# Optimization experiments

Hardware: AMD Instinct MI355X
Metric: run time of the kernel (lower is better)

The kernel has to match this reference:

```python
import jax, jax.numpy as jnp
import numpy as np

EPS = 1e-12  # matches torch.nn.functional.normalize default eps
TOP_K = 5


def _l2_normalize(x):
    n = jnp.linalg.norm(x, axis=-1, keepdims=True)
    return x / jnp.maximum(n, EPS)


def setup_inputs() -> dict:
    key = jax.random.key(0)
    k1, k2, k3 = jax.random.split(key, 3)
    B, S, D = 64, 128, 256
    CAP = 500000
    return {
        "query": jax.random.normal(k1, (B, S, D), dtype=jnp.float32),
        "memory_keys": jax.random.normal(k2, (CAP, D), dtype=jnp.float32),
        "memory_values": jax.random.normal(k3, (CAP, D), dtype=jnp.float32),
        "access_counts": jnp.zeros((CAP,), dtype=jnp.float32),
    }


def reference(query, memory_keys, memory_values, access_counts):
    # 3D query -> mean over sequence dim
    if query.ndim == 3:
        query = query.mean(axis=1)  # [B, D]
    q_norm = _l2_normalize(query)            # [B, D]
    k_norm = _l2_normalize(memory_keys)      # [CAP, D]
    sims = q_norm @ k_norm.T                 # [B, CAP] cosine similarities
    _, top_idx = jax.lax.top_k(sims, TOP_K)  # [B, 5]
    # gather top-k values and mean over k -> [B, D]
    retrieved = memory_values[top_idx].mean(axis=1)
    # scatter-add access counts (buffer side-effect in torch, returned here)
    new_counts = access_counts.at[top_idx.reshape(-1)].add(1.0)
    return retrieved, new_counts
```

## Files before the change

### kernel.cpp

```cpp
#include <hip/hip_runtime.h>
#include <math.h>

#define NQ    64
#define DIM   256
#define SEQ   128
#define CAP   500000
#define TOPK  5
#define KT    32
#define NTILE (CAP / KT)
#define NBLK  1024
#define PB    5
#define NC    (NBLK * PB)
#define DELTA 3.0e-3f
#define MAXC  192

typedef short short8v __attribute__((ext_vector_type(8)));
typedef float f32x4   __attribute__((ext_vector_type(4)));

#define SYNC_NODRAIN() do {                                        \
    asm volatile("s_waitcnt lgkmcnt(0)" ::: "memory");             \
    __builtin_amdgcn_s_barrier();                                  \
    asm volatile("" ::: "memory"); } while (0)

__device__ inline unsigned pkbf(float a, float b) {
    unsigned ua = __builtin_bit_cast(unsigned, a);
    unsigned ub = __builtin_bit_cast(unsigned, b);
    ua = (ua + 0x7fffu + ((ua >> 16) & 1u)) >> 16;
    ub = (ub + 0x7fffu + ((ub >> 16) & 1u)) >> 16;
    return ua | (ub << 16);
}

__global__ void qmean_part_kernel(const float* __restrict__ query,
                                  const float* __restrict__ ac,
                                  float* __restrict__ qpart,
                                  float* __restrict__ outCnt) {
    int blk = blockIdx.x;
    int d = threadIdx.x;
    int b = blk >> 2, ch = blk & 3;
    const float* qb = query + ((size_t)b * SEQ + ch * 32) * DIM;
    float s = 0.f;
    #pragma unroll 4
    for (int t = 0; t < 32; ++t) s += qb[(size_t)t * DIM + d];
    qpart[blk * DIM + d] = s;
    for (int i = blk * 256 + d; i < CAP / 4; i += 256 * 256)
        ((float4*)outCnt)[i] = ((const float4*)ac)[i];
}

__global__ void qmean_norm2_kernel(const float* __restrict__ qpart,
                                   float* __restrict__ qn) {
    int b = blockIdx.x;
    int d = threadIdx.x;
    float s = qpart[(b * 4 + 0) * DIM + d] + qpart[(b * 4 + 1) * DIM + d]
            + qpart[(b * 4 + 2) * DIM + d] + qpart[(b * 4 + 3) * DIM + d];
    float m = s * (1.0f / SEQ);
    float ss = m * m;
    #pragma unroll
    for (int off = 32; off > 0; off >>= 1) ss += __shfl_down(ss, off, 64);
    __shared__ float red[4];
    if ((threadIdx.x & 63) == 0) red[threadIdx.x >> 6] = ss;
    __syncthreads();
    float tot = red[0] + red[1] + red[2] + red[3];
    float r = 1.0f / fmaxf(sqrtf(tot), 1e-12f);
    qn[b * DIM + d] = m * r;
}

__global__ __launch_bounds__(256, 4) void sims_mfma_topk(
        const float* __restrict__ keys, const float* __restrict__ qn,
        float* __restrict__ candV, int* __restrict__ candI) {
    __shared__ __align__(16) unsigned short kb[2][KT * DIM];

    const int tid  = threadIdx.x;
    const int lane = tid & 63;
    const int wave = tid >> 6;
    const int key0 = lane & 15;
    const int g    = lane >> 4;
    const int kl3  = key0 & 7;

    short8v afr[8];
    {
        const float* qrow = qn + ((wave << 4) + key0) * DIM;
        int kbase = g * 8;
        #pragma unroll
        for (int st = 0; st < 8; ++st) {
            float4 a = *(const float4*)(qrow + st * 32 + kbase);
            float4 b = *(const float4*)(qrow + st * 32 + kbase + 4);
            uint4 w;
            w.x = pkbf(a.x, a.y); w.y = pkbf(a.z, a.w);
            w.z = pkbf(b.x, b.y); w.w = pkbf(b.z, b.w);
            afr[st] = __builtin_bit_cast(short8v, w);
        }
    }

    float tv[PB]; int ti[PB];
    #pragma unroll
    for (int p = 0; p < PB; ++p) { tv[p] = -INFINITY; ti[p] = 0; }

    f32x4 s0[8];
    auto issue_into = [&](int tile) {
        const f32x4* src = (const f32x4*)(keys + (size_t)tile * KT * DIM
                         + (size_t)(wave * 8) * DIM) + lane;
        #pragma unroll
        for (int j = 0; j < 8; ++j)
            s0[j] = __builtin_nontemporal_load(src + j * (DIM / 4));
    };
    auto write_stage = [&](int buf) {
        char* kc = (char*)&kb[buf][0];
        #pragma unroll
        for (int j = 0; j < 8; ++j) {
            uint2 pk;
            pk.x = pkbf(s0[j][0], s0[j][1]);
            pk.y = pkbf(s0[j][2], s0[j][3]);
            unsigned dst = (unsigned)((wave * 8 + j) * 512
                                      + ((lane * 8) ^ (j << 4)));
            *(uint2*)(kc + dst) = pk;
        }
    };

    auto body = [&](int tile, int cur) {
        f32x4 acc0  = {0.f, 0.f, 0.f, 0.f}, acc1  = {0.f, 0.f, 0.f, 0.f};
        f32x4 acck0 = {0.f, 0.f, 0.f, 0.f}, acck1 = {0.f, 0.f, 0.f, 0.f};
        const char* kc = (const char*)&kb[cur][0];
        #pragma unroll
        for (int st = 0; st < 8; ++st) {
            unsigned Xs = ((unsigned)(st * 64 + g * 16)) ^ (kl3 << 4);
            short8v b0 = *(const short8v*)(kc + key0 * 512 + Xs);
            short8v b1 = *(const short8v*)(kc + key0 * 512 + 8192 + Xs);
            acc0  = __builtin_amdgcn_mfma_f32_16x16x32_bf16(afr[st], b0, acc0, 0, 0, 0);
            acc1  = __builtin_amdgcn_mfma_f32_16x16x32_bf16(afr[st], b1, acc1, 0, 0, 0);
            acck0 = __builtin_amdgcn_mfma_f32_16x16x32_bf16(b0, b0, acck0, 0, 0, 0);
            acck1 = __builtin_amdgcn_mfma_f32_16x16x32_bf16(b1, b1, acck1, 0, 0, 0);
        }
        float dv0 = (key0 & 2) ? ((key0 & 1) ? acck0[3] : acck0[2])
                               : ((key0 & 1) ? acck0[1] : acck0[0]);
        float dv1 = (key0 & 2) ? ((key0 & 1) ? acck1[3] : acck1[2])
                               : ((key0 & 1) ? acck1[1] : acck1[0]);
        int src = ((key0 >> 2) << 4) + key0;
        float rk0 = __shfl(rsqrtf(fmaxf(dv0, 1e-24f)), src, 64);
        float rk1 = __shfl(rsqrtf(fmaxf(dv1, 1e-24f)), src, 64);
        SYNC_NODRAIN();

        float* simsp = (float*)&kb[cur][0];
        {
            int q0 = (wave << 4) + (g << 2);
            #pragma unroll
            for (int r = 0; r < 4; ++r) {
                simsp[(q0 + r) * 33 + key0]      = acc0[r] * rk0;
                simsp[(q0 + r) * 33 + 16 + key0] = acc1[r] * rk1;
            }
        }
        if (tile + NBLK < NTILE) write_stage(cur ^ 1);
        if (tile + 2 * NBLK < NTILE) issue_into(tile + 2 * NBLK);
        SYNC_NODRAIN();

        #pragma unroll
        for (int ks = 0; ks < 8; ++ks) {
            int ko = (wave << 3) + ks;
            float v = simsp[lane * 33 + ko];
            if (v > tv[PB - 1]) {
                tv[PB - 1] = v; ti[PB - 1] = tile * KT + ko;
                #pragma unroll
                for (int p = PB - 1; p > 0; --p) {
                    if (tv[p] > tv[p - 1]) {
                        float fv = tv[p]; tv[p] = tv[p - 1]; tv[p - 1] = fv;
                        int   fi = ti[p]; ti[p] = ti[p - 1]; ti[p - 1] = fi;
                    }
                }
            }
        }
    };

    int tile = blockIdx.x;
    issue_into(tile);
    write_stage(0);
    issue_into(tile + NBLK);
    SYNC_NODRAIN();

    int cur = 0;
    while (true) {
        body(tile, cur);
        tile += NBLK; cur ^= 1;
        if (tile >= NTILE) break;
    }

    __syncthreads();
    float* mv = (float*)&kb[0][0];
    int*   mi = (int*)&kb[0][0] + 2048;
    {
        int base = (wave * 64 + lane) * PB;
        #pragma unroll
        for (int p = 0; p < PB; ++p) { mv[base + p] = tv[p]; mi[base + p] = ti[p]; }
    }
    __syncthreads();
    if (wave == 0) {
        float fv[PB]; int fi[PB];
        #pragma unroll
        for (int p = 0; p < PB; ++p) { fv[p] = -INFINITY; fi[p] = 0; }
        for (int w = 0; w < 4; ++w) {
            #pragma unroll
            for (int p = 0; p < PB; ++p) {
                float v = mv[(w * 64 + lane) * PB + p];
                int  id = mi[(w * 64 + lane) * PB + p];
                if (v > fv[PB - 1]) {
                    fv[PB - 1] = v; fi[PB - 1] = id;
                    #pragma unroll
                    for (int p2 = PB - 1; p2 > 0; --p2) {
                        if (fv[p2] > fv[p2 - 1]) {
                            float a = fv[p2]; fv[p2] = fv[p2 - 1]; fv[p2 - 1] = a;
                            int   c = fi[p2]; fi[p2] = fi[p2 - 1]; fi[p2 - 1] = c;
                        }
                    }
                }
            }
        }
        size_t cb = ((size_t)lane * NBLK + blockIdx.x) * PB;
        #pragma unroll
        for (int p = 0; p < PB; ++p) { candV[cb + p] = fv[p]; candI[cb + p] = fi[p]; }
    }
}

__global__ void finalize_kernel(const float* __restrict__ candV,
                                const int* __restrict__ candI,
                                const float* __restrict__ keys,
                                const float* __restrict__ qn,
                                const float* __restrict__ values,
                                float* __restrict__ outRet,
                                float* __restrict__ outCnt) {
    const int b = blockIdx.x;
    const int t = threadIdx.x;
    const int lane = t & 63, wave = t >> 6;
    __shared__ float rv[256]; __shared__ int rp[256];
    __shared__ int   chosen[TOPK];
    __shared__ float v5s;
    __shared__ int   clist[MAXC];
    __shared__ float rsc[MAXC];
    __shared__ int   ccnt;
    __shared__ float qs[DIM];
    __shared__ int   kidx[TOPK];

    const float* cv = candV + (size_t)b * NC;
    const int*   ci = candI + (size_t)b * NC;

    for (int pass = 0; pass < TOPK; ++pass) {
        float lv = -INFINITY; int lp = 0x7fffffff;
        for (int m = t; m < NC; m += 256) {
            bool skip = false;
            for (int k2 = 0; k2 < pass; ++k2) skip |= (m == chosen[k2]);
            float v = cv[m];
            if (!skip && (v > lv || (v == lv && m < lp))) { lv = v; lp = m; }
        }
        rv[t] = lv; rp[t] = lp;
        __syncthreads();
        for (int s = 128; s > 0; s >>= 1) {
            if (t < s) {
                if (rv[t + s] > rv[t] || (rv[t + s] == rv[t] && rp[t + s] < rp[t])) {
                    rv[t] = rv[t + s]; rp[t] = rp[t + s];
                }
            }
            __syncthreads();
        }
        if (t == 0) { chosen[pass] = rp[0]; if (pass == TOPK - 1) v5s = rv[0]; }
        __syncthreads();
    }

    if (t == 0) ccnt = 0;
    __syncthreads();
    float thr = v5s - DELTA;
    for (int m = t; m < NC; m += 256) {
        if (cv[m] >= thr) {
            int pos = atomicAdd(&ccnt, 1);
            if (pos < MAXC) clist[pos] = ci[m];
        }
    }
    qs[t] = qn[b * DIM + t];
    __syncthreads();
    int cnt = min(ccnt, MAXC);

    for (int c = wave; c < cnt; c += 4) {
        const float4 k4 = *(const float4*)(keys + (size_t)clist[c] * DIM + lane * 4);
        const float4 q4 = *(const float4*)(qs + lane * 4);
        float d  = q4.x * k4.x + q4.y * k4.y + q4.z * k4.z + q4.w * k4.w;
        float s2 = k4.x * k4.x + k4.y * k4.y + k4.z * k4.z + k4.w * k4.w;
        #pragma unroll
        for (int off = 1; off < 64; off <<= 1) {
            d  += __shfl_xor(d, off, 64);
            s2 += __shfl_xor(s2, off, 64);
        }
        if (lane == 0) rsc[c] = d * rsqrtf(fmaxf(s2, 1e-24f));
    }
    __syncthreads();

    for (int pass = 0; pass < TOPK; ++pass) {
        float lv = -INFINITY; int lp = 0x7fffffff;
        if (t < cnt) {
            bool skip = false;
            for (int k2 = 0; k2 < pass; ++k2) skip |= (t == chosen[k2]);
            if (!skip) { lv = rsc[t]; lp = t; }
        }
        rv[t] = lv; rp[t] = lp;
        __syncthreads();
        for (int s = 128; s > 0; s >>= 1) {
            if (t < s) {
                if (rv[t + s] > rv[t] || (rv[t + s] == rv[t] && rp[t + s] < rp[t])) {
                    rv[t] = rv[t + s]; rp[t] = rp[t + s];
                }
            }
            __syncthreads();
        }
        if (t == 0) { chosen[pass] = rp[0]; kidx[pass] = clist[rp[0]]; }
        __syncthreads();
    }

    float s = 0.f;
    #pragma unroll
    for (int p = 0; p < TOPK; ++p) s += values[(size_t)kidx[p] * DIM + t];
    outRet[b * DIM + t] = s * 0.2f;
    if (t < TOPK) atomicAdd(&outCnt[kidx[t]], 1.0f);
}

extern "C" void kernel_launch(void* const* d_in, const int* in_sizes, int n_in,
                              void* d_out, int out_size, void* d_ws, size_t ws_size,
                              hipStream_t stream) {
    const float* query  = (const float*)d_in[0];
    const float* keys   = (const float*)d_in[1];
    const float* values = (const float*)d_in[2];
    const float* acnt   = (const float*)d_in[3];
    float* outRet = (float*)d_out;
    float* outCnt = outRet + NQ * DIM;

    char* ws = (char*)d_ws;
    float* qn    = (float*)ws;
    float* qpart = (float*)(ws + 65536);
    float* candV = (float*)(ws + 65536 + 262144);
    int*   candI = (int*)(ws + 65536 + 262144 + (size_t)NQ * NC * 4);

    qmean_part_kernel<<<256, 256, 0, stream>>>(query, acnt, qpart, outCnt);
    qmean_norm2_kernel<<<NQ, 256, 0, stream>>>(qpart, qn);
    sims_mfma_topk<<<NBLK, 256, 0, stream>>>(keys, qn, candV, candI);
    finalize_kernel<<<NQ, 256, 0, stream>>>(candV, candI, keys, qn, values,
                                            outRet, outCnt);
}
```

Baseline: 154.7 us.

## Deepen global-load prefetch to two register stages with fewer, larger blocks

Adds a second register staging buffer so each block keeps two tiles of key loads in flight instead of one, and unrolls the main loop by two to alternate between the buffers. Grid size drops from 1024 to 768 blocks, occupancy hint from 4 to 3 blocks per CU, and per-thread candidate list grows from 5 to 7 entries. The aim is to hide HBM latency for the streaming key reads, at the cost of extra register pressure and fewer resident waves.

```diff
diff --git a/kernel.cpp b/kernel.cpp
--- a/kernel.cpp
+++ b/kernel.cpp
@@ -8,8 +8,8 @@
 #define TOPK  5
 #define KT    32
 #define NTILE (CAP / KT)
-#define NBLK  1024
-#define PB    5
+#define NBLK  768
+#define PB    7
 #define NC    (NBLK * PB)
 #define DELTA 3.0e-3f
 #define MAXC  192
@@ -64,7 +64,7 @@
     qn[b * DIM + d] = m * r;
 }
 
-__global__ __launch_bounds__(256, 4) void sims_mfma_topk(
+__global__ __launch_bounds__(256, 3) void sims_mfma_topk(
         const float* __restrict__ keys, const float* __restrict__ qn,
         float* __restrict__ candV, int* __restrict__ candI) {
     __shared__ __align__(16) unsigned short kb[2][KT * DIM];
@@ -95,28 +95,28 @@
     #pragma unroll
     for (int p = 0; p < PB; ++p) { tv[p] = -INFINITY; ti[p] = 0; }
 
-    f32x4 s0[8];
-    auto issue_into = [&](int tile) {
+    f32x4 s0[8], s1[8];
+    auto issue_into = [&](f32x4 (&dst)[8], int tile) {
         const f32x4* src = (const f32x4*)(keys + (size_t)tile * KT * DIM
                          + (size_t)(wave * 8) * DIM) + lane;
         #pragma unroll
         for (int j = 0; j < 8; ++j)
-            s0[j] = __builtin_nontemporal_load(src + j * (DIM / 4));
+            dst[j] = __builtin_nontemporal_load(src + j * (DIM / 4));
     };
-    auto write_stage = [&](int buf) {
+    auto write_stage_from = [&](int buf, f32x4 (&stg)[8]) {
         char* kc = (char*)&kb[buf][0];
         #pragma unroll
         for (int j = 0; j < 8; ++j) {
             uint2 pk;
-            pk.x = pkbf(s0[j][0], s0[j][1]);
-            pk.y = pkbf(s0[j][2], s0[j][3]);
+            pk.x = pkbf(stg[j][0], stg[j][1]);
+            pk.y = pkbf(stg[j][2], stg[j][3]);
             unsigned dst = (unsigned)((wave * 8 + j) * 512
                                       + ((lane * 8) ^ (j << 4)));
             *(uint2*)(kc + dst) = pk;
         }
     };
 
-    auto body = [&](int tile, int cur) {
+    auto body = [&](int tile, int cur, f32x4 (&sc)[8]) {
         f32x4 acc0  = {0.f, 0.f, 0.f, 0.f}, acc1  = {0.f, 0.f, 0.f, 0.f};
         f32x4 acck0 = {0.f, 0.f, 0.f, 0.f}, acck1 = {0.f, 0.f, 0.f, 0.f};
         const char* kc = (const char*)&kb[cur][0];
@@ -148,8 +148,8 @@
                 simsp[(q0 + r) * 33 + 16 + key0] = acc1[r] * rk1;
             }
         }
-        if (tile + NBLK < NTILE) write_stage(cur ^ 1);
-        if (tile + 2 * NBLK < NTILE) issue_into(tile + 2 * NBLK);
+        if (tile + NBLK < NTILE) write_stage_from(cur ^ 1, sc);
+        if (tile + 3 * NBLK < NTILE) issue_into(sc, tile + 3 * NBLK);
         SYNC_NODRAIN();
 
         #pragma unroll
@@ -170,14 +170,18 @@
     };
 
     int tile = blockIdx.x;
-    issue_into(tile);
-    write_stage(0);
-    issue_into(tile + NBLK);
+    issue_into(s0, tile);
+    write_stage_from(0, s0);
+    issue_into(s1, tile + NBLK);
+    issue_into(s0, tile + 2 * NBLK);
     SYNC_NODRAIN();
 
     int cur = 0;
     while (true) {
-        body(tile, cur);
+        body(tile, cur, s1);
+        tile += NBLK; cur ^= 1;
+        if (tile >= NTILE) break;
+        body(tile, cur, s0);
         tile += NBLK; cur ^= 1;
         if (tile >= NTILE) break;
     }
```

Result: slower. 161.3 us (+4.3%).
